# Performance work log

Hardware: AMD Instinct MI355X
Metric: run time of the kernel (lower is better)

The kernel has to match this reference:

```python
import jax, jax.numpy as jnp
import numpy as np

KSZ = 7
PAD = 3


def setup_inputs() -> dict:
    key = jax.random.key(0)
    ks = jax.random.split(key, 5)
    b, t, c, h, w = 8, 16, 256, 28, 28
    x = jax.random.normal(ks[0], (b, t, c, h, w), dtype=jnp.float32)
    W1 = jax.random.normal(ks[1], (2 * t, t), dtype=jnp.float32) * 0.1
    W2 = jax.random.normal(ks[2], (KSZ, 2 * t), dtype=jnp.float32) * 0.1
    Wl1 = jax.random.normal(ks[3], (c // 4, c, KSZ), dtype=jnp.float32) * 0.05
    Wl2 = jax.random.normal(ks[4], (c, c // 4, 1), dtype=jnp.float32) * 0.1
    return {"x": x, "W1": W1, "W2": W2, "Wl1": Wl1, "Wl2": Wl2}


def _tam_forward(x, W1, W2, Wl1, Wl2):
    b, t, c, h, w = x.shape
    xp = jnp.transpose(x, (0, 2, 1, 3, 4))  # [b,c,t,h,w]
    pooled = jnp.mean(xp, axis=(3, 4))       # [b,c,t] (adaptive_avg_pool2d to 1x1)

    # G branch: per-(b,c) dynamic 7-tap softmax kernel
    g = jnp.tanh(jnp.einsum('bct,ut->bcu', pooled, W1))
    kernel = jax.nn.softmax(jnp.einsum('bcu,ku->bck', g, W2), axis=-1)  # [b,c,7]

    # L branch: conv1d(c -> c/4, k=7, pad=3) -> tanh -> conv1d(c/4 -> c, k=1) -> sigmoid
    y = jax.lax.conv_general_dilated(
        pooled, Wl1, window_strides=(1,), padding=[(PAD, PAD)],
        dimension_numbers=('NCH', 'OIH', 'NCH'))
    y = jnp.tanh(y)  # [b, c/4, t]
    local = jax.nn.sigmoid(jnp.einsum('oi,bit->bot', Wl2[:, :, 0], y))  # [b,c,t]

    gated = xp * local[:, :, :, None, None]  # [b,c,t,h,w]

    # Depthwise temporal conv (groups = b*c), stride 1, pad 3 on t
    padded = jnp.pad(gated, ((0, 0), (0, 0), (PAD, PAD), (0, 0), (0, 0)))
    out = jnp.zeros_like(gated)
    for k in range(KSZ):
        out = out + kernel[:, :, k, None, None, None] * padded[:, :, k:k + t]
    out = jnp.transpose(out, (0, 2, 1, 3, 4))  # [b,t,c,h,w]
    return out.reshape(b * t, c, h, w)


def reference(x, W1, W2, Wl1, Wl2):
    return _tam_forward(x, W1, W2, Wl1, Wl2)
```

## Files before the change

kernel.cpp:

```cpp
#include <hip/hip_runtime.h>

constexpr int B_  = 8;
constexpr int T_  = 16;
constexpr int C_  = 256;
constexpr int HW_ = 784;
constexpr int CO_ = 64;
constexpr int K_  = 7;
constexpr int U2_ = 32;

__global__ __launch_bounds__(256) void pool_kernel(const float* __restrict__ x,
                                                   float* __restrict__ pooled) {
    int bid  = blockIdx.x;
    int cg   = bid & 63;
    int bt   = bid >> 6;
    int t    = bt & 15;
    int b    = bt >> 4;
    int wave = threadIdx.x >> 6;
    int lane = threadIdx.x & 63;
    int c    = cg * 4 + wave;

    const float4* p4 = (const float4*)(x + ((size_t)bt * C_ + c) * HW_);
    float s = 0.f;
    for (int j = lane; j < 196; j += 64) {
        float4 v = p4[j];
        s += (v.x + v.y) + (v.z + v.w);
    }
#pragma unroll
    for (int m = 32; m >= 1; m >>= 1) s += __shfl_xor(s, m, 64);
    if (lane == 0) pooled[((size_t)b * C_ + c) * T_ + t] = s * (1.0f / 784.0f);
}

__global__ __launch_bounds__(256) void ty_kernel(const float* __restrict__ pooled,
                                                 const float* __restrict__ Wl1,
                                                 float* __restrict__ ty) {
    int b = blockIdx.x / CO_;
    int o = blockIdx.x % CO_;
    __shared__ float pld[T_ * 257];

    int tid = threadIdx.x;
    for (int idx = tid; idx < C_ * T_; idx += 256) {
        int i  = idx >> 4;
        int tt = idx & 15;
        pld[tt * 257 + i] = pooled[((size_t)b * C_ + i) * T_ + tt];
    }
    __syncthreads();

    int t = tid >> 4;
    int q = tid & 15;
    const float* wrow = Wl1 + (size_t)o * (C_ * K_);
    float acc = 0.f;
    for (int j = 0; j < 16; ++j) {
        int i = j * 16 + q;
        const float* wp = wrow + i * K_;
#pragma unroll
        for (int k = 0; k < K_; ++k) {
            int tt = t + k - 3;
            if (tt >= 0 && tt < T_) acc += wp[k] * pld[tt * 257 + i];
        }
    }
    acc += __shfl_xor(acc, 1, 64);
    acc += __shfl_xor(acc, 2, 64);
    acc += __shfl_xor(acc, 4, 64);
    acc += __shfl_xor(acc, 8, 64);
    if (q == 0) ty[((size_t)b * CO_ + o) * T_ + t] = tanhf(acc);
}

__global__ __launch_bounds__(256) void tam_main_kernel(const float* __restrict__ x,
                                                       const float* __restrict__ pooled,
                                                       const float* __restrict__ ty,
                                                       const float* __restrict__ W1,
                                                       const float* __restrict__ W2,
                                                       const float* __restrict__ Wl2,
                                                       float* __restrict__ out) {
    int bc = blockIdx.x;
    int b  = bc >> 8;
    int c  = bc & 255;
    int tid = threadIdx.x;

    __shared__ float loc_s[T_];
    __shared__ float g_s[U2_];
    __shared__ float s_s[K_];
    __shared__ float kw_s[K_];
    __shared__ float A_s[T_ * T_];

    {
        int t = tid >> 4, q = tid & 15;
        float acc = 0.f;
#pragma unroll
        for (int jj = 0; jj < 4; ++jj) {
            int o = q + jj * 16;
            acc += Wl2[(size_t)c * CO_ + o] * ty[((size_t)b * CO_ + o) * T_ + t];
        }
        acc += __shfl_xor(acc, 1, 64);
        acc += __shfl_xor(acc, 2, 64);
        acc += __shfl_xor(acc, 4, 64);
        acc += __shfl_xor(acc, 8, 64);
        if (q == 0) loc_s[t] = 1.0f / (1.0f + __expf(-acc));
    }
    if (tid < U2_) {
        float acc = 0.f;
#pragma unroll
        for (int t2 = 0; t2 < T_; ++t2)
            acc += pooled[((size_t)b * C_ + c) * T_ + t2] * W1[tid * T_ + t2];
        g_s[tid] = tanhf(acc);
    }
    __syncthreads();
    if (tid < K_) {
        float acc = 0.f;
#pragma unroll
        for (int u = 0; u < U2_; ++u) acc += g_s[u] * W2[tid * U2_ + u];
        s_s[tid] = acc;
    }
    __syncthreads();
    if (tid == 0) {
        float m = s_s[0];
#pragma unroll
        for (int k = 1; k < K_; ++k) m = fmaxf(m, s_s[k]);
        float e[K_], sum = 0.f;
#pragma unroll
        for (int k = 0; k < K_; ++k) { e[k] = __expf(s_s[k] - m); sum += e[k]; }
        float inv = 1.0f / sum;
#pragma unroll
        for (int k = 0; k < K_; ++k) kw_s[k] = e[k] * inv;
    }
    __syncthreads();
    {
        int t = tid >> 4, tp = tid & 15;
        int d = tp - t + 3;
        A_s[tid] = (d >= 0 && d < K_) ? kw_s[d] * loc_s[tp] : 0.f;
    }
    __syncthreads();

    if (tid < 196) {
        size_t base = ((size_t)(b * T_) * C_ + c) * HW_;
        const size_t tstride = (size_t)C_ * HW_;

        float4 xv[T_];
#pragma unroll
        for (int tp = 0; tp < T_; ++tp) {
            const float4* xp = (const float4*)(x + base + (size_t)tp * tstride);
            xv[tp] = xp[tid];
        }
#pragma unroll
        for (int t = 0; t < T_; ++t) {
            float4 acc = make_float4(0.f, 0.f, 0.f, 0.f);
#pragma unroll
            for (int d = -3; d <= 3; ++d) {
                int tp = t + d;
                if (tp >= 0 && tp < T_) {
                    float a = A_s[t * T_ + tp];
                    acc.x += a * xv[tp].x;
                    acc.y += a * xv[tp].y;
                    acc.z += a * xv[tp].z;
                    acc.w += a * xv[tp].w;
                }
            }
            float4* op = (float4*)(out + base + (size_t)t * tstride);
            op[tid] = acc;
        }
    }
}

extern "C" void kernel_launch(void* const* d_in, const int* in_sizes, int n_in,
                              void* d_out, int out_size, void* d_ws, size_t ws_size,
                              hipStream_t stream) {
    const float* x   = (const float*)d_in[0];
    const float* W1  = (const float*)d_in[1];
    const float* W2  = (const float*)d_in[2];
    const float* Wl1 = (const float*)d_in[3];
    const float* Wl2 = (const float*)d_in[4];
    float* out = (float*)d_out;

    float* pooled = (float*)d_ws;
    float* ty     = pooled + B_ * C_ * T_;

    pool_kernel<<<B_ * T_ * (C_ / 4), 256, 0, stream>>>(x, pooled);
    ty_kernel<<<B_ * CO_, 256, 0, stream>>>(pooled, Wl1, ty);
    tam_main_kernel<<<B_ * C_, 256, 0, stream>>>(x, pooled, ty, W1, W2, Wl2, out);
}
```

Baseline: 71.84 us.

## Split per-channel parameter build from a flat streaming conv kernel

Moves the per-(b,c) softmax kernel and local gate computation into a separate small single-wave kernel that writes a compact parameter row. The main pass becomes a flat grid where every thread handles one float4 column, so the 60 idle threads of each old 256-thread block no longer sit out the streaming loop. It also applies the gate on load and uses nontemporal stores. The cost is an extra kernel launch and a small round trip of the parameters through global memory.

```diff
diff --git a/kernel.cpp b/kernel.cpp
--- a/kernel.cpp
+++ b/kernel.cpp
@@ -7,6 +7,8 @@
 constexpr int CO_ = 64;
 constexpr int K_  = 7;
 constexpr int U2_ = 32;
+
+typedef float floatx4 __attribute__((ext_vector_type(4)));
 
 __global__ __launch_bounds__(256) void pool_kernel(const float* __restrict__ x,
                                                    float* __restrict__ pooled) {
@@ -65,54 +67,50 @@
     if (q == 0) ty[((size_t)b * CO_ + o) * T_ + t] = tanhf(acc);
 }
 
-__global__ __launch_bounds__(256) void tam_main_kernel(const float* __restrict__ x,
-                                                       const float* __restrict__ pooled,
-                                                       const float* __restrict__ ty,
-                                                       const float* __restrict__ W1,
-                                                       const float* __restrict__ W2,
-                                                       const float* __restrict__ Wl2,
-                                                       float* __restrict__ out) {
+__global__ __launch_bounds__(64) void abuild_kernel(const float* __restrict__ pooled,
+                                                    const float* __restrict__ ty,
+                                                    const float* __restrict__ W1,
+                                                    const float* __restrict__ W2,
+                                                    const float* __restrict__ Wl2,
+                                                    float* __restrict__ P) {
     int bc = blockIdx.x;
     int b  = bc >> 8;
     int c  = bc & 255;
-    int tid = threadIdx.x;
+    int lane = threadIdx.x;
 
-    __shared__ float loc_s[T_];
     __shared__ float g_s[U2_];
     __shared__ float s_s[K_];
-    __shared__ float kw_s[K_];
-    __shared__ float A_s[T_ * T_];
+    __shared__ float loc_s[T_];
+    __shared__ float kw_s[8];
 
     {
-        int t = tid >> 4, q = tid & 15;
+        int t = lane >> 2, q = lane & 3;
         float acc = 0.f;
 #pragma unroll
-        for (int jj = 0; jj < 4; ++jj) {
-            int o = q + jj * 16;
-            acc += Wl2[(size_t)c * CO_ + o] * ty[((size_t)b * CO_ + o) * T_ + t];
+        for (int jj = 0; jj < 16; ++jj) {
+            int i = q * 16 + jj;
+            acc += Wl2[(size_t)c * CO_ + i] * ty[((size_t)b * CO_ + i) * T_ + t];
         }
         acc += __shfl_xor(acc, 1, 64);
         acc += __shfl_xor(acc, 2, 64);
-        acc += __shfl_xor(acc, 4, 64);
-        acc += __shfl_xor(acc, 8, 64);
         if (q == 0) loc_s[t] = 1.0f / (1.0f + __expf(-acc));
     }
-    if (tid < U2_) {
+    if (lane < U2_) {
         float acc = 0.f;
 #pragma unroll
         for (int t2 = 0; t2 < T_; ++t2)
-            acc += pooled[((size_t)b * C_ + c) * T_ + t2] * W1[tid * T_ + t2];
-        g_s[tid] = tanhf(acc);
+            acc += pooled[((size_t)b * C_ + c) * T_ + t2] * W1[lane * T_ + t2];
+        g_s[lane] = tanhf(acc);
     }
     __syncthreads();
-    if (tid < K_) {
+    if (lane < K_) {
         float acc = 0.f;
 #pragma unroll
-        for (int u = 0; u < U2_; ++u) acc += g_s[u] * W2[tid * U2_ + u];
-        s_s[tid] = acc;
+        for (int u = 0; u < U2_; ++u) acc += g_s[u] * W2[lane * U2_ + u];
+        s_s[lane] = acc;
     }
     __syncthreads();
-    if (tid == 0) {
+    if (lane == 0) {
         float m = s_s[0];
 #pragma unroll
         for (int k = 1; k < K_; ++k) m = fmaxf(m, s_s[k]);
@@ -122,42 +120,61 @@
         float inv = 1.0f / sum;
 #pragma unroll
         for (int k = 0; k < K_; ++k) kw_s[k] = e[k] * inv;
+        kw_s[7] = 0.f;
     }
     __syncthreads();
-    {
-        int t = tid >> 4, tp = tid & 15;
-        int d = tp - t + 3;
-        A_s[tid] = (d >= 0 && d < K_) ? kw_s[d] * loc_s[tp] : 0.f;
+    float* row = P + (size_t)bc * 32;
+    if (lane < 8)                 row[lane] = kw_s[lane];
+    if (lane >= 8 && lane < 24)   row[lane] = loc_s[lane - 8];
+}
+
+__global__ __launch_bounds__(256) void stream_kernel(const float* __restrict__ x,
+                                                     const float* __restrict__ P,
+                                                     float* __restrict__ out) {
+    int gid = blockIdx.x * 256 + threadIdx.x;
+    int bc  = gid / 196;
+    int col = gid - bc * 196;
+    int b   = bc >> 8;
+    int c   = bc & 255;
+
+    const float* row = P + (size_t)bc * 32;
+    float4 kwa = *(const float4*)(row);
+    float4 kwb = *(const float4*)(row + 4);
+    float kw[K_] = {kwa.x, kwa.y, kwa.z, kwa.w, kwb.x, kwb.y, kwb.z};
+    float loc[T_];
+#pragma unroll
+    for (int j = 0; j < 4; ++j) {
+        float4 l = *(const float4*)(row + 8 + 4 * j);
+        loc[4 * j + 0] = l.x; loc[4 * j + 1] = l.y;
+        loc[4 * j + 2] = l.z; loc[4 * j + 3] = l.w;
     }
-    __syncthreads();
 
-    if (tid < 196) {
-        size_t base = ((size_t)(b * T_) * C_ + c) * HW_;
-        const size_t tstride = (size_t)C_ * HW_;
+    size_t base = ((size_t)(b * T_) * C_ + c) * HW_ + (size_t)col * 4;
+    const size_t ts = (size_t)C_ * HW_;
 
-        float4 xv[T_];
+    float4 yv[T_];
 #pragma unroll
-        for (int tp = 0; tp < T_; ++tp) {
-            const float4* xp = (const float4*)(x + base + (size_t)tp * tstride);
-            xv[tp] = xp[tid];
+    for (int tp = 0; tp < T_; ++tp) {
+        float4 v = *(const float4*)(x + base + tp * ts);
+        float l = loc[tp];
+        v.x *= l; v.y *= l; v.z *= l; v.w *= l;
+        yv[tp] = v;
+    }
+#pragma unroll
+    for (int t = 0; t < T_; ++t) {
+        floatx4 acc = {0.f, 0.f, 0.f, 0.f};
+#pragma unroll
+        for (int d = -3; d <= 3; ++d) {
+            int tp = t + d;
+            if (tp >= 0 && tp < T_) {
+                float a = kw[d + 3];
+                acc.x += a * yv[tp].x;
+                acc.y += a * yv[tp].y;
+                acc.z += a * yv[tp].z;
+                acc.w += a * yv[tp].w;
+            }
         }
-#pragma unroll
-        for (int t = 0; t < T_; ++t) {
-            float4 acc = make_float4(0.f, 0.f, 0.f, 0.f);
-#pragma unroll
-            for (int d = -3; d <= 3; ++d) {
-                int tp = t + d;
-                if (tp >= 0 && tp < T_) {
-                    float a = A_s[t * T_ + tp];
-                    acc.x += a * xv[tp].x;
-                    acc.y += a * xv[tp].y;
-                    acc.z += a * xv[tp].z;
-                    acc.w += a * xv[tp].w;
-                }
-            }
-            float4* op = (float4*)(out + base + (size_t)t * tstride);
-            op[tid] = acc;
-        }
+        __builtin_nontemporal_store(acc, (floatx4*)(out + base + (size_t)t * ts));
     }
 }
 
@@ -173,8 +190,10 @@
 
     float* pooled = (float*)d_ws;
     float* ty     = pooled + B_ * C_ * T_;
+    float* P      = ty + B_ * CO_ * T_;
 
     pool_kernel<<<B_ * T_ * (C_ / 4), 256, 0, stream>>>(x, pooled);
     ty_kernel<<<B_ * CO_, 256, 0, stream>>>(pooled, Wl1, ty);
-    tam_main_kernel<<<B_ * C_, 256, 0, stream>>>(x, pooled, ty, W1, W2, Wl2, out);
+    abuild_kernel<<<B_ * C_, 64, 0, stream>>>(pooled, ty, W1, W2, Wl2, P);
+    stream_kernel<<<(B_ * C_ * 196) / 256, 256, 0, stream>>>(x, P, out);
 }
```

Result: no change. 72.72 us (+1.2%).

## Prefetch x before coefficient math, use rolling register window and nontemporal stores

Applied to the files above, without the earlier changes.

The main kernel now issues loads for the first 11 time steps of x before computing the gating and softmax coefficients, so memory latency overlaps the small coefficient computation. The 16x16 banded A matrix in shared memory is dropped. Coefficients are read once into scalar registers via readfirstlane, x is pre-scaled by the local gate, and the band is applied directly. Output is written in two halves with a rolling register window and nontemporal stores. This lowers register pressure and avoids polluting the cache with output, but adds a second load phase mid-kernel.

```diff
diff --git a/kernel.cpp b/kernel.cpp
--- a/kernel.cpp
+++ b/kernel.cpp
@@ -7,6 +7,12 @@
 constexpr int CO_ = 64;
 constexpr int K_  = 7;
 constexpr int U2_ = 32;
+
+typedef float floatx4 __attribute__((ext_vector_type(4)));
+
+__device__ __forceinline__ float rfl(float v) {
+    return __int_as_float(__builtin_amdgcn_readfirstlane(__float_as_int(v)));
+}
 
 __global__ __launch_bounds__(256) void pool_kernel(const float* __restrict__ x,
                                                    float* __restrict__ pooled) {
@@ -19,10 +25,10 @@
     int lane = threadIdx.x & 63;
     int c    = cg * 4 + wave;
 
-    const float4* p4 = (const float4*)(x + ((size_t)bt * C_ + c) * HW_);
+    const floatx4* p4 = (const floatx4*)(x + ((size_t)bt * C_ + c) * HW_);
     float s = 0.f;
     for (int j = lane; j < 196; j += 64) {
-        float4 v = p4[j];
+        floatx4 v = p4[j];
         s += (v.x + v.y) + (v.z + v.w);
     }
 #pragma unroll
@@ -65,23 +71,35 @@
     if (q == 0) ty[((size_t)b * CO_ + o) * T_ + t] = tanhf(acc);
 }
 
-__global__ __launch_bounds__(256) void tam_main_kernel(const float* __restrict__ x,
-                                                       const float* __restrict__ pooled,
-                                                       const float* __restrict__ ty,
-                                                       const float* __restrict__ W1,
-                                                       const float* __restrict__ W2,
-                                                       const float* __restrict__ Wl2,
-                                                       float* __restrict__ out) {
+__global__ __launch_bounds__(256) void stream_coef_kernel(const float* __restrict__ x,
+                                                          const float* __restrict__ pooled,
+                                                          const float* __restrict__ ty,
+                                                          const float* __restrict__ W1,
+                                                          const float* __restrict__ W2,
+                                                          const float* __restrict__ Wl2,
+                                                          float* __restrict__ out) {
     int bc = blockIdx.x;
     int b  = bc >> 8;
     int c  = bc & 255;
     int tid = threadIdx.x;
+    bool active = tid < 196;
+
+    const size_t chan = ((size_t)(b * T_) * C_ + c) * HW_ + (size_t)tid * 4;
+    const float* xb = x + chan;
+    float*       ob = out + chan;
+    const size_t ts = (size_t)C_ * HW_;
+
+    floatx4 w[11];
+    if (active) {
+#pragma unroll
+        for (int tp = 0; tp < 11; ++tp)
+            w[tp] = *(const floatx4*)(xb + (size_t)tp * ts);
+    }
 
     __shared__ float loc_s[T_];
     __shared__ float g_s[U2_];
-    __shared__ float s_s[K_];
-    __shared__ float kw_s[K_];
-    __shared__ float A_s[T_ * T_];
+    __shared__ float s_s[8];
+    __shared__ float kw_s[8];
 
     {
         int t = tid >> 4, q = tid & 15;
@@ -101,7 +119,7 @@
         float acc = 0.f;
 #pragma unroll
         for (int t2 = 0; t2 < T_; ++t2)
-            acc += pooled[((size_t)b * C_ + c) * T_ + t2] * W1[tid * T_ + t2];
+            acc += pooled[(size_t)bc * T_ + t2] * W1[tid * T_ + t2];
         g_s[tid] = tanhf(acc);
     }
     __syncthreads();
@@ -124,40 +142,44 @@
         for (int k = 0; k < K_; ++k) kw_s[k] = e[k] * inv;
     }
     __syncthreads();
-    {
-        int t = tid >> 4, tp = tid & 15;
-        int d = tp - t + 3;
-        A_s[tid] = (d >= 0 && d < K_) ? kw_s[d] * loc_s[tp] : 0.f;
-    }
-    __syncthreads();
-
-    if (tid < 196) {
-        size_t base = ((size_t)(b * T_) * C_ + c) * HW_;
-        const size_t tstride = (size_t)C_ * HW_;
-
-        float4 xv[T_];
-#pragma unroll
-        for (int tp = 0; tp < T_; ++tp) {
-            const float4* xp = (const float4*)(x + base + (size_t)tp * tstride);
-            xv[tp] = xp[tid];
-        }
-#pragma unroll
-        for (int t = 0; t < T_; ++t) {
-            float4 acc = make_float4(0.f, 0.f, 0.f, 0.f);
-#pragma unroll
-            for (int d = -3; d <= 3; ++d) {
-                int tp = t + d;
-                if (tp >= 0 && tp < T_) {
-                    float a = A_s[t * T_ + tp];
-                    acc.x += a * xv[tp].x;
-                    acc.y += a * xv[tp].y;
-                    acc.z += a * xv[tp].z;
-                    acc.w += a * xv[tp].w;
-                }
-            }
-            float4* op = (float4*)(out + base + (size_t)t * tstride);
-            op[tid] = acc;
-        }
+
+    float kw[K_], lc[T_];
+#pragma unroll
+    for (int k = 0; k < K_; ++k) kw[k] = rfl(kw_s[k]);
+#pragma unroll
+    for (int t = 0; t < T_; ++t) lc[t] = rfl(loc_s[t]);
+
+    if (!active) return;
+
+#pragma unroll
+    for (int tp = 0; tp < 11; ++tp) w[tp] *= lc[tp];
+
+#pragma unroll
+    for (int t = 0; t < 8; ++t) {
+        floatx4 acc = {0.f, 0.f, 0.f, 0.f};
+#pragma unroll
+        for (int d = -3; d <= 3; ++d) {
+            int tp = t + d;
+            if (tp >= 0 && tp <= 10) acc += kw[d + 3] * w[tp];
+        }
+        __builtin_nontemporal_store(acc, (floatx4*)(ob + (size_t)t * ts));
+    }
+
+#pragma unroll
+    for (int j = 0; j < 6; ++j) w[j] = w[5 + j];
+#pragma unroll
+    for (int tp = 11; tp < 16; ++tp)
+        w[tp - 5] = *(const floatx4*)(xb + (size_t)tp * ts) * lc[tp];
+
+#pragma unroll
+    for (int t = 8; t < 16; ++t) {
+        floatx4 acc = {0.f, 0.f, 0.f, 0.f};
+#pragma unroll
+        for (int d = -3; d <= 3; ++d) {
+            int tp = t + d;
+            if (tp <= 15) acc += kw[d + 3] * w[tp - 5];
+        }
+        __builtin_nontemporal_store(acc, (floatx4*)(ob + (size_t)t * ts));
     }
 }
 
@@ -176,5 +198,5 @@
 
     pool_kernel<<<B_ * T_ * (C_ / 4), 256, 0, stream>>>(x, pooled);
     ty_kernel<<<B_ * CO_, 256, 0, stream>>>(pooled, Wl1, ty);
-    tam_main_kernel<<<B_ * C_, 256, 0, stream>>>(x, pooled, ty, W1, W2, Wl2, out);
-}
+    stream_coef_kernel<<<B_ * C_, 256, 0, stream>>>(x, pooled, ty, W1, W2, Wl2, out);
+}
```

Result: faster. 68.66 us (-4.4%).
